# Performance work log

Measured on AMD Instinct MI355X. Metric: run time of the kernel, lower is better.

## Reference

```python
import jax, jax.numpy as jnp
import numpy as np

E = 8192      # number of original edges -> artificial nodes
N = 2048      # number of original graph nodes (id range)
C_IN = 128
C_OUT = 128
NEG_SLOPE = 0.2


def setup_inputs() -> dict:
    key = jax.random.key(0)
    k1, k2, k3, k4, k5 = jax.random.split(key, 5)
    x = jax.random.normal(k1, (E, C_IN), dtype=jnp.float32)
    edge_index = jax.random.randint(k2, (2, E), 0, N, dtype=jnp.int64)
    # GATConv params (heads=1): linear weight, attention vectors, bias
    W = jax.random.normal(k3, (C_IN, C_OUT), dtype=jnp.float32) / np.sqrt(C_IN)
    att_src = jax.random.normal(k4, (C_OUT,), dtype=jnp.float32) / np.sqrt(C_OUT)
    att_dst = jax.random.normal(k5, (C_OUT,), dtype=jnp.float32) / np.sqrt(C_OUT)
    bias = jnp.zeros((C_OUT,), dtype=jnp.float32)
    return {"x": x, "edge_index": edge_index, "W": W,
            "att_src": att_src, "att_dst": att_dst, "bias": bias}


def reference(x, edge_index, W, att_src, att_dst, bias):
    # --- line-graph construction (vectorized version of the O(E^2) loop) ---
    s = edge_index[0]  # [E] source node of each original edge
    d = edge_index[1]  # [E] target node of each original edge
    share = ((s[:, None] == s[None, :]) | (s[:, None] == d[None, :]) |
             (d[:, None] == s[None, :]) | (d[:, None] == d[None, :]))  # [E,E]
    eye = jnp.eye(x.shape[0], dtype=bool)
    # original loop only adds pairs i != j (symmetrically); GATConv then adds self loops
    adj = (share & ~eye) | eye  # adj[i, j]: message j -> i allowed

    # --- GATConv (heads=1, concat) over the dense line-graph adjacency ---
    h = x @ W                       # [E, C_OUT]
    a_src = h @ att_src             # [E] per-source attention logit
    a_dst = h @ att_dst             # [E] per-target attention logit
    scores = a_dst[:, None] + a_src[None, :]          # [E,E], row=target, col=source
    scores = jax.nn.leaky_relu(scores, NEG_SLOPE)
    scores = jnp.where(adj, scores, -jnp.inf)
    alpha = jax.nn.softmax(scores, axis=1)            # softmax over source edges per target
    out = alpha @ h + bias          # [E, C_OUT]
    return out
```

## Files before the change

kernel.cpp:

```cpp
#include <hip/hip_runtime.h>

#define E 8192
#define NNODE 2048
#define C 128
#define CAPN 32

typedef unsigned int u32;
typedef unsigned long long u64;

__global__ __launch_bounds__(256) void gat_prep(
    const float* __restrict__ x, const float* __restrict__ W,
    const float* __restrict__ att_s, const float* __restrict__ att_d,
    const int* __restrict__ ei,
    float* __restrict__ h, float* __restrict__ asrc, float* __restrict__ adst,
    int* __restrict__ packed, int* __restrict__ cnt, int* __restrict__ nlist)
{
    const int tid = threadIdx.x, lane = tid & 63, wv = tid >> 6;
    const int g = blockIdx.x * 256 + tid;
    if (g < E) {
        const int s = ei[g], d = ei[E + g];
        packed[g] = (s << 16) | d;
        int slot = atomicAdd(&cnt[s], 1);
        if (slot < CAPN) nlist[s * CAPN + slot] = g;
        if (d != s) {
            slot = atomicAdd(&cnt[d], 1);
            if (slot < CAPN) nlist[d * CAPN + slot] = g;
        }
    }

    const int row0 = blockIdx.x * 16 + wv * 4;
    __shared__ __align__(16) float xs[4][4][C];
    #pragma unroll
    for (int r = 0; r < 4; ++r)
        *reinterpret_cast<float2*>(&xs[wv][r][2 * lane]) =
            *reinterpret_cast<const float2*>(&x[(size_t)(row0 + r) * C + 2 * lane]);
    __syncthreads();

    float a00 = 0.f, a01 = 0.f, a10 = 0.f, a11 = 0.f;
    float a20 = 0.f, a21 = 0.f, a30 = 0.f, a31 = 0.f;
    const float4* xp0 = reinterpret_cast<const float4*>(xs[wv][0]);
    const float4* xp1 = reinterpret_cast<const float4*>(xs[wv][1]);
    const float4* xp2 = reinterpret_cast<const float4*>(xs[wv][2]);
    const float4* xp3 = reinterpret_cast<const float4*>(xs[wv][3]);
    const float* Wc = W + 2 * lane;

#define ROWFMA(V, A0, A1)                                    \
    A0 = fmaf(V.x, w0.x, A0); A1 = fmaf(V.x, w0.y, A1);      \
    A0 = fmaf(V.y, w1.x, A0); A1 = fmaf(V.y, w1.y, A1);      \
    A0 = fmaf(V.z, w2.x, A0); A1 = fmaf(V.z, w2.y, A1);      \
    A0 = fmaf(V.w, w3.x, A0); A1 = fmaf(V.w, w3.y, A1);

    for (int k4 = 0; k4 < C / 4; ++k4) {
        const float4 v0 = xp0[k4], v1 = xp1[k4], v2 = xp2[k4], v3 = xp3[k4];
        const float2 w0 = *reinterpret_cast<const float2*>(Wc + (4 * k4 + 0) * C);
        const float2 w1 = *reinterpret_cast<const float2*>(Wc + (4 * k4 + 1) * C);
        const float2 w2 = *reinterpret_cast<const float2*>(Wc + (4 * k4 + 2) * C);
        const float2 w3 = *reinterpret_cast<const float2*>(Wc + (4 * k4 + 3) * C);
        ROWFMA(v0, a00, a01)
        ROWFMA(v1, a10, a11)
        ROWFMA(v2, a20, a21)
        ROWFMA(v3, a30, a31)
    }
#undef ROWFMA

    const float2 asv = *reinterpret_cast<const float2*>(att_s + 2 * lane);
    const float2 adv = *reinterpret_cast<const float2*>(att_d + 2 * lane);
#define EPI(R, A0, A1) {                                                        \
    *reinterpret_cast<float2*>(&h[(size_t)(row0 + R) * C + 2 * lane]) =         \
        make_float2(A0, A1);                                                    \
    float ps = fmaf(A0, asv.x, A1 * asv.y);                                     \
    float pd = fmaf(A0, adv.x, A1 * adv.y);                                     \
    _Pragma("unroll")                                                           \
    for (int off = 32; off > 0; off >>= 1) {                                    \
        ps += __shfl_xor(ps, off); pd += __shfl_xor(pd, off);                   \
    }                                                                           \
    if (lane == 0) { asrc[row0 + R] = ps; adst[row0 + R] = pd; } }
    EPI(0, a00, a01)
    EPI(1, a10, a11)
    EPI(2, a20, a21)
    EPI(3, a30, a31)
#undef EPI
}

__global__ __launch_bounds__(256) void gat_aggr(
    const int* __restrict__ packed, const float* __restrict__ h,
    const float* __restrict__ asrc, const float* __restrict__ adst,
    const float* __restrict__ bias,
    const int* __restrict__ cnt, const int* __restrict__ nlist,
    float* __restrict__ out)
{
    __shared__ float2 lst[4][64];
    const int tid = threadIdx.x, lane = tid & 63, wv = tid >> 6;
    const int i = blockIdx.x * 4 + wv;

    const u32 pi = (u32)packed[i];
    const u32 si = pi >> 16, di = pi & 0xffffu;
    const float adi = adst[i];
    int len_s = cnt[si]; if (len_s > CAPN) len_s = CAPN;
    int len_d = (di == si) ? 0 : cnt[di]; if (len_d > CAPN) len_d = CAPN;
    const int ntot = len_s + len_d;

    int key = 0x7fffffff, jg = 0;
    float sc = -INFINITY;
    bool valid = false;
    if (lane < ntot) {
        const bool from_s = lane < len_s;
        const int idx = from_s ? ((int)si * CAPN + lane)
                               : ((int)di * CAPN + (lane - len_s));
        const int j = nlist[idx];
        const u32 pj = (u32)packed[j];
        valid = from_s || ((pj >> 16) != si && (pj & 0xffffu) != si);
        if (valid) {
            const float s0 = adi + asrc[j];
            sc = s0 >= 0.f ? s0 : 0.2f * s0;
            key = j; jg = j;
        }
    }

    float m = sc;
    #pragma unroll
    for (int off = 32; off > 0; off >>= 1) m = fmaxf(m, __shfl_xor(m, off));
    const int nvalid = (int)__popcll(__ballot(valid));

    #pragma unroll
    for (int k = 2; k <= 64; k <<= 1) {
        #pragma unroll
        for (int st = k >> 1; st > 0; st >>= 1) {
            const int   ok = __shfl_xor(key, st);
            const int   oj = __shfl_xor(jg, st);
            const float os = __shfl_xor(sc, st);
            const bool takeMin = ((lane & k) == 0) == ((lane & st) == 0);
            const bool takeOther = takeMin ? (ok < key) : (ok > key);
            if (takeOther) { key = ok; jg = oj; sc = os; }
        }
    }
    lst[wv][lane] = make_float2(__int_as_float(jg), sc);

    float lsum = 0.f, o0 = 0.f, o1 = 0.f;
    for (int t = 0; t < nvalid; ++t) {
        const float2 e = lst[wv][t];
        const float p = __expf(e.y - m);
        const int j = __float_as_int(e.x);
        lsum += p;
        const float2 hv = *reinterpret_cast<const float2*>(&h[(size_t)j * C + 2 * lane]);
        o0 = fmaf(p, hv.x, o0);
        o1 = fmaf(p, hv.y, o1);
    }
    const float inv = 1.0f / lsum;
    const float2 bv = *reinterpret_cast<const float2*>(bias + 2 * lane);
    *reinterpret_cast<float2*>(&out[(size_t)i * C + 2 * lane]) =
        make_float2(fmaf(o0, inv, bv.x), fmaf(o1, inv, bv.y));
}

extern "C" void kernel_launch(void* const* d_in, const int* in_sizes, int n_in,
                              void* d_out, int out_size, void* d_ws, size_t ws_size,
                              hipStream_t stream) {
    const float* x     = (const float*)d_in[0];
    const int*   ei    = (const int*)d_in[1];
    const float* W     = (const float*)d_in[2];
    const float* att_s = (const float*)d_in[3];
    const float* att_d = (const float*)d_in[4];
    const float* bias  = (const float*)d_in[5];

    float* h      = (float*)d_ws;
    float* asrc   = h + (size_t)E * C;
    float* adst   = asrc + E;
    int*   packed = (int*)(adst + E);
    int*   cnt    = packed + E;
    int*   nlist  = cnt + NNODE;

    hipMemsetAsync(cnt, 0, NNODE * sizeof(int), stream);
    gat_prep<<<E / 16, 256, 0, stream>>>(x, W, att_s, att_d, ei,
                                         h, asrc, adst, packed, cnt, nlist);
    gat_aggr<<<E / 4, 256, 0, stream>>>(packed, h, asrc, adst, bias,
                                        cnt, nlist, (float*)d_out);
}
```

Measured before the change: 38.28 us.

## Build adjacency lists in shared-memory blocks, retile GEMM, precompute softmax weights

The memset is removed: 8 dedicated blocks each scan all edges and build neighbour lists for their slice of nodes, using shared-memory atomic counters. The remaining blocks compute h with 32 rows per block and W staged through shared memory. Bias is folded into h, which is valid because the softmax weights sum to one. The aggregation kernel computes exp before the bitonic sort so it shuffles fewer values, and unrolls the gather four edges at a time, padding unused slots with p=0. The trade-off is that each index block reads all 8192 edges, and list order within a node still depends on atomic order.

```diff
diff --git a/kernel.cpp b/kernel.cpp
--- a/kernel.cpp
+++ b/kernel.cpp
@@ -4,6 +4,10 @@
 #define NNODE 2048
 #define C 128
 #define CAPN 32
+#define NIDX 8
+#define NPI (NNODE / NIDX)
+#define RPB 32
+#define NGEMM (E / RPB)
 
 typedef unsigned int u32;
 typedef unsigned long long u64;
@@ -11,81 +15,114 @@
 __global__ __launch_bounds__(256) void gat_prep(
     const float* __restrict__ x, const float* __restrict__ W,
     const float* __restrict__ att_s, const float* __restrict__ att_d,
-    const int* __restrict__ ei,
+    const float* __restrict__ bias, const int* __restrict__ ei,
     float* __restrict__ h, float* __restrict__ asrc, float* __restrict__ adst,
     int* __restrict__ packed, int* __restrict__ cnt, int* __restrict__ nlist)
 {
-    const int tid = threadIdx.x, lane = tid & 63, wv = tid >> 6;
-    const int g = blockIdx.x * 256 + tid;
-    if (g < E) {
-        const int s = ei[g], d = ei[E + g];
-        packed[g] = (s << 16) | d;
-        int slot = atomicAdd(&cnt[s], 1);
-        if (slot < CAPN) nlist[s * CAPN + slot] = g;
-        if (d != s) {
-            slot = atomicAdd(&cnt[d], 1);
-            if (slot < CAPN) nlist[d * CAPN + slot] = g;
-        }
-    }
-
-    const int row0 = blockIdx.x * 16 + wv * 4;
-    __shared__ __align__(16) float xs[4][4][C];
+    __shared__ __align__(16) float smem[8192];
+    const int tid = threadIdx.x;
+
+    if (blockIdx.x < NIDX) {
+        int* lcnt = (int*)smem;
+        const int lo = (int)blockIdx.x * NPI;
+        if (tid < NPI) lcnt[tid] = 0;
+        __syncthreads();
+        for (int g = tid; g < E; g += 256) {
+            const int s = ei[g], d = ei[E + g];
+            if ((g >> 10) == (int)blockIdx.x)
+                packed[g] = (s << 16) | d;
+            const int sl = s - lo, dl = d - lo;
+            if ((unsigned)sl < NPI) {
+                const int slot = atomicAdd(&lcnt[sl], 1);
+                if (slot < CAPN) nlist[s * CAPN + slot] = g;
+            }
+            if (d != s && (unsigned)dl < NPI) {
+                const int slot = atomicAdd(&lcnt[dl], 1);
+                if (slot < CAPN) nlist[d * CAPN + slot] = g;
+            }
+        }
+        __syncthreads();
+        if (tid < NPI) cnt[lo + tid] = lcnt[tid];
+        return;
+    }
+
+    float* xs = smem;
+    float* wt = smem + 4096;
+    const int lane = tid & 63, wv = tid >> 6;
+    const int row0 = ((int)blockIdx.x - NIDX) * RPB;
+
     #pragma unroll
-    for (int r = 0; r < 4; ++r)
-        *reinterpret_cast<float2*>(&xs[wv][r][2 * lane]) =
-            *reinterpret_cast<const float2*>(&x[(size_t)(row0 + r) * C + 2 * lane]);
-    __syncthreads();
-
-    float a00 = 0.f, a01 = 0.f, a10 = 0.f, a11 = 0.f;
-    float a20 = 0.f, a21 = 0.f, a30 = 0.f, a31 = 0.f;
-    const float4* xp0 = reinterpret_cast<const float4*>(xs[wv][0]);
-    const float4* xp1 = reinterpret_cast<const float4*>(xs[wv][1]);
-    const float4* xp2 = reinterpret_cast<const float4*>(xs[wv][2]);
-    const float4* xp3 = reinterpret_cast<const float4*>(xs[wv][3]);
-    const float* Wc = W + 2 * lane;
-
-#define ROWFMA(V, A0, A1)                                    \
-    A0 = fmaf(V.x, w0.x, A0); A1 = fmaf(V.x, w0.y, A1);      \
-    A0 = fmaf(V.y, w1.x, A0); A1 = fmaf(V.y, w1.y, A1);      \
-    A0 = fmaf(V.z, w2.x, A0); A1 = fmaf(V.z, w2.y, A1);      \
-    A0 = fmaf(V.w, w3.x, A0); A1 = fmaf(V.w, w3.y, A1);
-
-    for (int k4 = 0; k4 < C / 4; ++k4) {
-        const float4 v0 = xp0[k4], v1 = xp1[k4], v2 = xp2[k4], v3 = xp3[k4];
-        const float2 w0 = *reinterpret_cast<const float2*>(Wc + (4 * k4 + 0) * C);
-        const float2 w1 = *reinterpret_cast<const float2*>(Wc + (4 * k4 + 1) * C);
-        const float2 w2 = *reinterpret_cast<const float2*>(Wc + (4 * k4 + 2) * C);
-        const float2 w3 = *reinterpret_cast<const float2*>(Wc + (4 * k4 + 3) * C);
-        ROWFMA(v0, a00, a01)
-        ROWFMA(v1, a10, a11)
-        ROWFMA(v2, a20, a21)
-        ROWFMA(v3, a30, a31)
-    }
-#undef ROWFMA
+    for (int u = 0; u < 4; ++u) {
+        const int f = tid + u * 256;
+        *reinterpret_cast<float4*>(&xs[f * 4]) =
+            *reinterpret_cast<const float4*>(&x[(size_t)row0 * C + f * 4]);
+    }
+
+    float a0x = 0.f, a0y = 0.f, a1x = 0.f, a1y = 0.f;
+    float a2x = 0.f, a2y = 0.f, a3x = 0.f, a3y = 0.f;
+    float a4x = 0.f, a4y = 0.f, a5x = 0.f, a5y = 0.f;
+    float a6x = 0.f, a6y = 0.f, a7x = 0.f, a7y = 0.f;
+    const float* xw = xs + (wv * 8) * C;
+
+    for (int kt = 0; kt < 4; ++kt) {
+        __syncthreads();
+        #pragma unroll
+        for (int u = 0; u < 4; ++u) {
+            const int f = tid + u * 256;
+            *reinterpret_cast<float4*>(&wt[f * 4]) =
+                *reinterpret_cast<const float4*>(&W[(size_t)kt * 32 * C + f * 4]);
+        }
+        __syncthreads();
+        const int kb = kt * 32;
+        #pragma unroll
+        for (int k4 = 0; k4 < 8; ++k4) {
+            float4 v0 = *reinterpret_cast<const float4*>(&xw[0 * C + kb + k4 * 4]);
+            float4 v1 = *reinterpret_cast<const float4*>(&xw[1 * C + kb + k4 * 4]);
+            float4 v2 = *reinterpret_cast<const float4*>(&xw[2 * C + kb + k4 * 4]);
+            float4 v3 = *reinterpret_cast<const float4*>(&xw[3 * C + kb + k4 * 4]);
+            float4 v4 = *reinterpret_cast<const float4*>(&xw[4 * C + kb + k4 * 4]);
+            float4 v5 = *reinterpret_cast<const float4*>(&xw[5 * C + kb + k4 * 4]);
+            float4 v6 = *reinterpret_cast<const float4*>(&xw[6 * C + kb + k4 * 4]);
+            float4 v7 = *reinterpret_cast<const float4*>(&xw[7 * C + kb + k4 * 4]);
+            const float2 w0 = *reinterpret_cast<const float2*>(&wt[(k4 * 4 + 0) * C + 2 * lane]);
+            const float2 w1 = *reinterpret_cast<const float2*>(&wt[(k4 * 4 + 1) * C + 2 * lane]);
+            const float2 w2 = *reinterpret_cast<const float2*>(&wt[(k4 * 4 + 2) * C + 2 * lane]);
+            const float2 w3 = *reinterpret_cast<const float2*>(&wt[(k4 * 4 + 3) * C + 2 * lane]);
+#define K4FMA(V, AX, AY)                                     \
+            AX = fmaf(V.x, w0.x, AX); AY = fmaf(V.x, w0.y, AY); \
+            AX = fmaf(V.y, w1.x, AX); AY = fmaf(V.y, w1.y, AY); \
+            AX = fmaf(V.z, w2.x, AX); AY = fmaf(V.z, w2.y, AY); \
+            AX = fmaf(V.w, w3.x, AX); AY = fmaf(V.w, w3.y, AY);
+            K4FMA(v0, a0x, a0y) K4FMA(v1, a1x, a1y)
+            K4FMA(v2, a2x, a2y) K4FMA(v3, a3x, a3y)
+            K4FMA(v4, a4x, a4y) K4FMA(v5, a5x, a5y)
+            K4FMA(v6, a6x, a6y) K4FMA(v7, a7x, a7y)
+#undef K4FMA
+        }
+    }
 
     const float2 asv = *reinterpret_cast<const float2*>(att_s + 2 * lane);
     const float2 adv = *reinterpret_cast<const float2*>(att_d + 2 * lane);
-#define EPI(R, A0, A1) {                                                        \
-    *reinterpret_cast<float2*>(&h[(size_t)(row0 + R) * C + 2 * lane]) =         \
-        make_float2(A0, A1);                                                    \
-    float ps = fmaf(A0, asv.x, A1 * asv.y);                                     \
-    float pd = fmaf(A0, adv.x, A1 * adv.y);                                     \
+    const float2 bv  = *reinterpret_cast<const float2*>(bias  + 2 * lane);
+    const int rw0 = row0 + wv * 8;
+#define EPI(R, AX, AY) {                                                        \
+    *reinterpret_cast<float2*>(&h[(size_t)(rw0 + R) * C + 2 * lane]) =          \
+        make_float2(AX + bv.x, AY + bv.y);              \
+    float ps = fmaf(AX, asv.x, AY * asv.y);                                     \
+    float pd = fmaf(AX, adv.x, AY * adv.y);                                     \
     _Pragma("unroll")                                                           \
     for (int off = 32; off > 0; off >>= 1) {                                    \
         ps += __shfl_xor(ps, off); pd += __shfl_xor(pd, off);                   \
     }                                                                           \
-    if (lane == 0) { asrc[row0 + R] = ps; adst[row0 + R] = pd; } }
-    EPI(0, a00, a01)
-    EPI(1, a10, a11)
-    EPI(2, a20, a21)
-    EPI(3, a30, a31)
+    if (lane == 0) { asrc[rw0 + R] = ps; adst[rw0 + R] = pd; } }
+    EPI(0, a0x, a0y) EPI(1, a1x, a1y) EPI(2, a2x, a2y) EPI(3, a3x, a3y)
+    EPI(4, a4x, a4y) EPI(5, a5x, a5y) EPI(6, a6x, a6y) EPI(7, a7x, a7y)
 #undef EPI
 }
 
 __global__ __launch_bounds__(256) void gat_aggr(
     const int* __restrict__ packed, const float* __restrict__ h,
     const float* __restrict__ asrc, const float* __restrict__ adst,
-    const float* __restrict__ bias,
     const int* __restrict__ cnt, const int* __restrict__ nlist,
     float* __restrict__ out)
 {
@@ -94,26 +131,24 @@
     const int i = blockIdx.x * 4 + wv;
 
     const u32 pi = (u32)packed[i];
-    const u32 si = pi >> 16, di = pi & 0xffffu;
+    const int si = (int)(pi >> 16), di = (int)(pi & 0xffffu);
     const float adi = adst[i];
     int len_s = cnt[si]; if (len_s > CAPN) len_s = CAPN;
     int len_d = (di == si) ? 0 : cnt[di]; if (len_d > CAPN) len_d = CAPN;
     const int ntot = len_s + len_d;
 
-    int key = 0x7fffffff, jg = 0;
+    int key = 0x7fffffff;
     float sc = -INFINITY;
     bool valid = false;
     if (lane < ntot) {
         const bool from_s = lane < len_s;
-        const int idx = from_s ? ((int)si * CAPN + lane)
-                               : ((int)di * CAPN + (lane - len_s));
-        const int j = nlist[idx];
+        const int j = nlist[(from_s ? si : di) * CAPN + (from_s ? lane : lane - len_s)];
         const u32 pj = (u32)packed[j];
-        valid = from_s || ((pj >> 16) != si && (pj & 0xffffu) != si);
+        valid = from_s || ((int)(pj >> 16) != si && (int)(pj & 0xffffu) != si);
         if (valid) {
             const float s0 = adi + asrc[j];
             sc = s0 >= 0.f ? s0 : 0.2f * s0;
-            key = j; jg = j;
+            key = j;
         }
     }
 
@@ -121,35 +156,42 @@
     #pragma unroll
     for (int off = 32; off > 0; off >>= 1) m = fmaxf(m, __shfl_xor(m, off));
     const int nvalid = (int)__popcll(__ballot(valid));
+
+    float p = __expf(sc - m);
 
     #pragma unroll
     for (int k = 2; k <= 64; k <<= 1) {
         #pragma unroll
         for (int st = k >> 1; st > 0; st >>= 1) {
             const int   ok = __shfl_xor(key, st);
-            const int   oj = __shfl_xor(jg, st);
-            const float os = __shfl_xor(sc, st);
+            const float op = __shfl_xor(p, st);
             const bool takeMin = ((lane & k) == 0) == ((lane & st) == 0);
-            const bool takeOther = takeMin ? (ok < key) : (ok > key);
-            if (takeOther) { key = ok; jg = oj; sc = os; }
-        }
-    }
-    lst[wv][lane] = make_float2(__int_as_float(jg), sc);
-
+            if (takeMin ? (ok < key) : (ok > key)) { key = ok; p = op; }
+        }
+    }
+    lst[wv][lane] = make_float2(__int_as_float(key == 0x7fffffff ? i : key), p);
+
+    const int nch = (nvalid + 3) >> 2;
     float lsum = 0.f, o0 = 0.f, o1 = 0.f;
-    for (int t = 0; t < nvalid; ++t) {
-        const float2 e = lst[wv][t];
-        const float p = __expf(e.y - m);
-        const int j = __float_as_int(e.x);
-        lsum += p;
-        const float2 hv = *reinterpret_cast<const float2*>(&h[(size_t)j * C + 2 * lane]);
-        o0 = fmaf(p, hv.x, o0);
-        o1 = fmaf(p, hv.y, o1);
+    const float* hb = h + 2 * lane;
+    for (int t = 0; t < nch; ++t) {
+        const float2 e0 = lst[wv][4 * t + 0];
+        const float2 e1 = lst[wv][4 * t + 1];
+        const float2 e2 = lst[wv][4 * t + 2];
+        const float2 e3 = lst[wv][4 * t + 3];
+        const float2 h0 = *reinterpret_cast<const float2*>(hb + (size_t)__float_as_int(e0.x) * C);
+        const float2 h1 = *reinterpret_cast<const float2*>(hb + (size_t)__float_as_int(e1.x) * C);
+        const float2 h2 = *reinterpret_cast<const float2*>(hb + (size_t)__float_as_int(e2.x) * C);
+        const float2 h3 = *reinterpret_cast<const float2*>(hb + (size_t)__float_as_int(e3.x) * C);
+        lsum += (e0.y + e1.y) + (e2.y + e3.y);
+        o0 = fmaf(e0.y, h0.x, o0); o1 = fmaf(e0.y, h0.y, o1);
+        o0 = fmaf(e1.y, h1.x, o0); o1 = fmaf(e1.y, h1.y, o1);
+        o0 = fmaf(e2.y, h2.x, o0); o1 = fmaf(e2.y, h2.y, o1);
+        o0 = fmaf(e3.y, h3.x, o0); o1 = fmaf(e3.y, h3.y, o1);
     }
     const float inv = 1.0f / lsum;
-    const float2 bv = *reinterpret_cast<const float2*>(bias + 2 * lane);
     *reinterpret_cast<float2*>(&out[(size_t)i * C + 2 * lane]) =
-        make_float2(fmaf(o0, inv, bv.x), fmaf(o1, inv, bv.y));
+        make_float2(o0 * inv, o1 * inv);
 }
 
 extern "C" void kernel_launch(void* const* d_in, const int* in_sizes, int n_in,
@@ -169,9 +211,8 @@
     int*   cnt    = packed + E;
     int*   nlist  = cnt + NNODE;
 
-    hipMemsetAsync(cnt, 0, NNODE * sizeof(int), stream);
-    gat_prep<<<E / 16, 256, 0, stream>>>(x, W, att_s, att_d, ei,
-                                         h, asrc, adst, packed, cnt, nlist);
-    gat_aggr<<<E / 4, 256, 0, stream>>>(packed, h, asrc, adst, bias,
-                                        cnt, nlist, (float*)d_out);
+    gat_prep<<<NIDX + NGEMM, 256, 0, stream>>>(x, W, att_s, att_d, bias, ei,
+                                               h, asrc, adst, packed, cnt, nlist);
+    gat_aggr<<<E / 4, 256, 0, stream>>>(packed, h, asrc, adst, cnt, nlist,
+                                        (float*)d_out);
 }
```

Result: slower. 45.20 us (+18.1%).
